# Kernel optimization log

Measured on AMD Instinct MI355X. Metric: run time of the kernel, lower is better.

Reference implementation:

```python
import jax, jax.numpy as jnp
import numpy as np

N_NODES = 100_000
N_EDGES = 1_600_000
IN_DIM = 64
OUT_DIM = 64
EPS = 1e-5


def setup_inputs() -> dict:
    key = jax.random.key(0)
    k1, k2, k3, k4, k5, k6 = jax.random.split(key, 6)
    node = jax.random.normal(k1, (N_NODES, 3), dtype=jnp.float32)
    features = jax.random.normal(k2, (N_NODES, IN_DIM), dtype=jnp.float32)
    # src column covers every node so torch.unique(edges[:,0]) == arange(N_NODES)
    src = (jnp.arange(N_EDGES, dtype=jnp.int64) % N_NODES)
    dst = jax.random.randint(k3, (N_EDGES,), 0, N_NODES, dtype=jnp.int64)
    edges = jnp.stack([src, dst], axis=1)
    # torch.nn.Linear weight: [out_dim, in_dim+3], no bias
    W = jax.random.normal(k4, (OUT_DIM, IN_DIM + 3), dtype=jnp.float32) / np.sqrt(IN_DIM + 3)
    gamma = jnp.ones((OUT_DIM,), dtype=jnp.float32)
    beta = jnp.zeros((OUT_DIM,), dtype=jnp.float32)
    return {"node": node, "features": features, "W": W, "gamma": gamma,
            "beta": beta, "edges": edges}


def reference(node, features, W, gamma, beta, edges):
    src = edges[:, 0]
    dst = edges[:, 1]
    # gather + concat: [E, in_dim + 3]
    msg = jnp.concatenate([features[dst], node[dst] - node[src]], axis=1)
    # linear (no bias): [E, out_dim]
    h = msg @ W.T
    # BatchNorm1d (training mode: biased batch statistics over E rows)
    mean = jnp.mean(h, axis=0)
    var = jnp.mean(jnp.square(h - mean), axis=0)
    h = (h - mean) * jax.lax.rsqrt(var + EPS) * gamma + beta
    h = jax.nn.relu(h)
    # scatter_reduce amax with include_self=True on a zeros tensor:
    # per-destination max, including the initial 0 (relu output >= 0 anyway)
    n = node.shape[0]
    pooled = jnp.zeros((n, h.shape[1]), dtype=features.dtype).at[src].max(h)
    return pooled
```

## Files before the change

kernel.cpp:

```cpp
#include <hip/hip_runtime.h>

#define N_NODES 100000
#define N_EDGES 1600000
#define EPS 1e-5f

typedef __bf16 bf16x8 __attribute__((ext_vector_type(8)));
typedef float  f32x4  __attribute__((ext_vector_type(4)));
typedef unsigned short u16x4 __attribute__((ext_vector_type(4)));

__device__ __forceinline__ unsigned short f2bf(float f) {
  return __builtin_bit_cast(unsigned short, static_cast<__bf16>(f));
}

__global__ __launch_bounds__(256) void prep_kernel(
    const float* __restrict__ feat, const float* __restrict__ W,
    unsigned short* __restrict__ featbf, unsigned short* __restrict__ Wbf) {
  int b = blockIdx.x, t = threadIdx.x;
  if (b < 6250) {
    int idx = (b * 256 + t) * 4;
    f32x4 v = *(const f32x4*)(feat + idx);
    u16x4 o;
    o[0] = f2bf(v[0]); o[1] = f2bf(v[1]); o[2] = f2bf(v[2]); o[3] = f2bf(v[3]);
    *(u16x4*)(featbf + idx) = o;
  } else {
    int wi = (b - 6250) * 256 + t;
    if (wi < 64 * 96) {
      int n = wi / 96, c = wi % 96;
      Wbf[wi] = (c < 67) ? f2bf(W[n * 67 + c]) : (unsigned short)0;
    }
  }
}

__global__ __launch_bounds__(256) void graph_kernel(
    const float* __restrict__ nodep, const int* __restrict__ edges,
    const unsigned short* __restrict__ featbf,
    const unsigned short* __restrict__ Wbf,
    float* __restrict__ maxv, float* __restrict__ minv,
    float* __restrict__ stats, int nwaves) {
  const int lane = threadIdx.x & 63;
  const int wave = (int)((blockIdx.x * blockDim.x + threadIdx.x) >> 6);
  const int c    = lane & 15;
  const int quad = lane >> 4;

  bf16x8 Bfrag[4][3];
#pragma unroll
  for (int t = 0; t < 4; ++t) {
    const unsigned short* wrow = Wbf + (t * 16 + c) * 96 + quad * 8;
#pragma unroll
    for (int s = 0; s < 3; ++s)
      Bfrag[t][s] = *(const bf16x8*)(wrow + s * 32);
  }

  float s1[4] = {0.f, 0.f, 0.f, 0.f};
  float s2[4] = {0.f, 0.f, 0.f, 0.f};

  for (int i = wave; i < N_NODES; i += nwaves) {
    int dst_own = 0;
    if (lane < 16) dst_own = edges[2 * (i + lane * N_NODES) + 1];
    int dst_m = __shfl(dst_own, c, 64);

    const unsigned short* frow = featbf + (size_t)dst_m * 64 + quad * 8;
    bf16x8 A0 = *(const bf16x8*)(frow);
    bf16x8 A1 = *(const bf16x8*)(frow + 32);

    bf16x8 A2;
#pragma unroll
    for (int j = 0; j < 8; ++j) A2[j] = (__bf16)0.0f;
    float nx = nodep[3 * i], ny = nodep[3 * i + 1], nz = nodep[3 * i + 2];
    if (quad == 0) {
      const float* dp = nodep + (size_t)dst_m * 3;
      A2[0] = (__bf16)(dp[0] - nx);
      A2[1] = (__bf16)(dp[1] - ny);
      A2[2] = (__bf16)(dp[2] - nz);
    }

    float mxw = 0.f, mnw = 0.f;
#pragma unroll
    for (int t = 0; t < 4; ++t) {
      f32x4 acc = {0.f, 0.f, 0.f, 0.f};
      acc = __builtin_amdgcn_mfma_f32_16x16x32_bf16(A0, Bfrag[t][0], acc, 0, 0, 0);
      acc = __builtin_amdgcn_mfma_f32_16x16x32_bf16(A1, Bfrag[t][1], acc, 0, 0, 0);
      acc = __builtin_amdgcn_mfma_f32_16x16x32_bf16(A2, Bfrag[t][2], acc, 0, 0, 0);

      float a0 = acc[0], a1 = acc[1], a2 = acc[2], a3 = acc[3];
      s1[t] += (a0 + a1) + (a2 + a3);
      s2[t] += (a0 * a0 + a1 * a1) + (a2 * a2 + a3 * a3);

      float mx = fmaxf(fmaxf(a0, a1), fmaxf(a2, a3));
      float mn = fminf(fminf(a0, a1), fminf(a2, a3));
      mx = fmaxf(mx, __shfl_xor(mx, 16, 64));
      mx = fmaxf(mx, __shfl_xor(mx, 32, 64));
      mn = fminf(mn, __shfl_xor(mn, 16, 64));
      mn = fminf(mn, __shfl_xor(mn, 32, 64));
      if (t == quad) { mxw = mx; mnw = mn; }
    }
    maxv[i * 64 + lane] = mxw;
    minv[i * 64 + lane] = mnw;
  }

#pragma unroll
  for (int t = 0; t < 4; ++t) {
    s1[t] += __shfl_xor(s1[t], 16, 64);
    s1[t] += __shfl_xor(s1[t], 32, 64);
    s2[t] += __shfl_xor(s2[t], 16, 64);
    s2[t] += __shfl_xor(s2[t], 32, 64);
  }
  float s1w = quad == 0 ? s1[0] : quad == 1 ? s1[1] : quad == 2 ? s1[2] : s1[3];
  float s2w = quad == 0 ? s2[0] : quad == 1 ? s2[1] : quad == 2 ? s2[2] : s2[3];
  stats[(size_t)lane * nwaves + wave]        = s1w;
  stats[(size_t)(64 + lane) * nwaves + wave] = s2w;
}

__global__ __launch_bounds__(256) void stats_kernel(
    const float* __restrict__ stats, const float* __restrict__ gamma,
    const float* __restrict__ beta, float* __restrict__ ss, int nwaves) {
  int d = blockIdx.x;
  int t = threadIdx.x;
  const float* r1 = stats + (size_t)d * nwaves;
  const float* r2 = stats + (size_t)(64 + d) * nwaves;
  float a = 0.f, b = 0.f;
  for (int k = t; k < nwaves; k += 256) { a += r1[k]; b += r2[k]; }
  __shared__ float l1[256], l2[256];
  l1[t] = a; l2[t] = b;
  __syncthreads();
  for (int s = 128; s > 0; s >>= 1) {
    if (t < s) { l1[t] += l1[t + s]; l2[t] += l2[t + s]; }
    __syncthreads();
  }
  if (t == 0) {
    const float inv_ne = 1.0f / (float)N_EDGES;
    float mean = l1[0] * inv_ne;
    float var  = fmaxf(l2[0] * inv_ne - mean * mean, 0.f);
    float sc   = gamma[d] * rsqrtf(var + EPS);
    ss[d]      = sc;
    ss[64 + d] = beta[d] - mean * sc;
  }
}

__global__ __launch_bounds__(256) void finalize_kernel(
    const float* __restrict__ minv, const float* __restrict__ ss,
    float* out) {
  int idx = blockIdx.x * 256 + threadIdx.x;
  int d = idx & 63;
  float sc = ss[d], sh = ss[64 + d];
  float v = (sc >= 0.f) ? out[idx] : minv[idx];
  out[idx] = fmaxf(fmaf(v, sc, sh), 0.f);
}

extern "C" void kernel_launch(void* const* d_in, const int* in_sizes, int n_in,
                              void* d_out, int out_size, void* d_ws, size_t ws_size,
                              hipStream_t stream) {
  const float* nodep = (const float*)d_in[0];
  const float* feat  = (const float*)d_in[1];
  const float* W     = (const float*)d_in[2];
  const float* gamma = (const float*)d_in[3];
  const float* beta  = (const float*)d_in[4];
  const int*   edges = (const int*)d_in[5];

  char* ws = (char*)d_ws;
  unsigned short* Wbf    = (unsigned short*)ws;
  unsigned short* featbf = (unsigned short*)(ws + 12288);
  float* minv  = (float*)(ws + 12288 + 12800000);
  float* stats = (float*)(ws + 12288 + 12800000 + 25600000);
  float* ss    = (float*)(ws + 12288 + 12800000 + 25600000 + 4194304);
  float* maxv  = (float*)d_out;

  const int nwaves = 8192;

  prep_kernel<<<6250 + 24, 256, 0, stream>>>(feat, W, featbf, Wbf);
  graph_kernel<<<nwaves / 4, 256, 0, stream>>>(nodep, edges, featbf, Wbf,
                                               maxv, minv, stats, nwaves);
  stats_kernel<<<64, 256, 0, stream>>>(stats, gamma, beta, ss, nwaves);
  finalize_kernel<<<25000, 256, 0, stream>>>(minv, ss, maxv);
}
```

Before: 178.2 us.

## Precompute per-node linear projection, then gather projected rows per edge

Uses linearity to compute W·[feat; pos] once per node (100k rows) into an fp16 table, then per edge gathers the projected row and subtracts W_pos·pos_src computed on the fly. This removes the per-edge MFMA GEMM and the separate bf16 feature conversion pass. The gather kernel also prefetches the next iteration's edge indices and reduces max/min/stats across lanes with shuffles. The risk is precision: the projection is stored in fp16 and the position difference is no longer rounded to bf16 before the multiply.

```diff
diff --git a/kernel.cpp b/kernel.cpp
--- a/kernel.cpp
+++ b/kernel.cpp
@@ -4,111 +4,152 @@
 #define N_EDGES 1600000
 #define EPS 1e-5f
 
-typedef __bf16 bf16x8 __attribute__((ext_vector_type(8)));
-typedef float  f32x4  __attribute__((ext_vector_type(4)));
-typedef unsigned short u16x4 __attribute__((ext_vector_type(4)));
-
-__device__ __forceinline__ unsigned short f2bf(float f) {
-  return __builtin_bit_cast(unsigned short, static_cast<__bf16>(f));
-}
-
-__global__ __launch_bounds__(256) void prep_kernel(
-    const float* __restrict__ feat, const float* __restrict__ W,
-    unsigned short* __restrict__ featbf, unsigned short* __restrict__ Wbf) {
-  int b = blockIdx.x, t = threadIdx.x;
-  if (b < 6250) {
-    int idx = (b * 256 + t) * 4;
-    f32x4 v = *(const f32x4*)(feat + idx);
-    u16x4 o;
-    o[0] = f2bf(v[0]); o[1] = f2bf(v[1]); o[2] = f2bf(v[2]); o[3] = f2bf(v[3]);
-    *(u16x4*)(featbf + idx) = o;
-  } else {
-    int wi = (b - 6250) * 256 + t;
-    if (wi < 64 * 96) {
-      int n = wi / 96, c = wi % 96;
-      Wbf[wi] = (c < 67) ? f2bf(W[n * 67 + c]) : (unsigned short)0;
-    }
-  }
-}
-
-__global__ __launch_bounds__(256) void graph_kernel(
+typedef __bf16    bf16x8 __attribute__((ext_vector_type(8)));
+typedef _Float16  f16x8  __attribute__((ext_vector_type(8)));
+typedef float     f32x4  __attribute__((ext_vector_type(4)));
+
+__global__ __launch_bounds__(256) void gemm_kernel(
+    const float* __restrict__ nodep, const float* __restrict__ feat,
+    const float* __restrict__ W, unsigned short* __restrict__ g) {
+  const int lane = threadIdx.x & 63;
+  const int wave = (int)((blockIdx.x * blockDim.x + threadIdx.x) >> 6);
+  const int c    = lane & 15;
+  const int quad = lane >> 4;
+  if (wave >= N_NODES / 16) return;
+
+  bf16x8 Bfrag[4][3];
+#pragma unroll
+  for (int t = 0; t < 4; ++t) {
+    const float* wrow = W + (t * 16 + c) * 67;
+#pragma unroll
+    for (int s = 0; s < 3; ++s) {
+#pragma unroll
+      for (int j = 0; j < 8; ++j) {
+        int k = s * 32 + quad * 8 + j;
+        Bfrag[t][s][j] = (k < 67) ? (__bf16)wrow[k] : (__bf16)0.0f;
+      }
+    }
+  }
+
+  const int v = wave * 16 + c;
+  const float* frow = feat + (size_t)v * 64 + quad * 8;
+  bf16x8 A0, A1;
+#pragma unroll
+  for (int j = 0; j < 8; ++j) {
+    A0[j] = (__bf16)frow[j];
+    A1[j] = (__bf16)frow[32 + j];
+  }
+  bf16x8 A2;
+#pragma unroll
+  for (int j = 0; j < 8; ++j) A2[j] = (__bf16)0.0f;
+  if (quad == 0) {
+    const float* np = nodep + (size_t)v * 3;
+    A2[0] = (__bf16)np[0];
+    A2[1] = (__bf16)np[1];
+    A2[2] = (__bf16)np[2];
+  }
+
+#pragma unroll
+  for (int t = 0; t < 4; ++t) {
+    f32x4 acc = {0.f, 0.f, 0.f, 0.f};
+    acc = __builtin_amdgcn_mfma_f32_16x16x32_bf16(A0, Bfrag[t][0], acc, 0, 0, 0);
+    acc = __builtin_amdgcn_mfma_f32_16x16x32_bf16(A1, Bfrag[t][1], acc, 0, 0, 0);
+    acc = __builtin_amdgcn_mfma_f32_16x16x32_bf16(A2, Bfrag[t][2], acc, 0, 0, 0);
+    unsigned short* gp = g + (size_t)(wave * 16 + quad * 4) * 64 + t * 16 + c;
+#pragma unroll
+    for (int r = 0; r < 4; ++r)
+      gp[r * 64] = __builtin_bit_cast(unsigned short, (_Float16)acc[r]);
+  }
+}
+
+__global__ __launch_bounds__(256) void gather_kernel(
     const float* __restrict__ nodep, const int* __restrict__ edges,
-    const unsigned short* __restrict__ featbf,
-    const unsigned short* __restrict__ Wbf,
+    const _Float16* __restrict__ g, const float* __restrict__ W,
     float* __restrict__ maxv, float* __restrict__ minv,
     float* __restrict__ stats, int nwaves) {
   const int lane = threadIdx.x & 63;
   const int wave = (int)((blockIdx.x * blockDim.x + threadIdx.x) >> 6);
-  const int c    = lane & 15;
-  const int quad = lane >> 4;
-
-  bf16x8 Bfrag[4][3];
-#pragma unroll
-  for (int t = 0; t < 4; ++t) {
-    const unsigned short* wrow = Wbf + (t * 16 + c) * 96 + quad * 8;
-#pragma unroll
-    for (int s = 0; s < 3; ++s)
-      Bfrag[t][s] = *(const bf16x8*)(wrow + s * 32);
-  }
-
-  float s1[4] = {0.f, 0.f, 0.f, 0.f};
-  float s2[4] = {0.f, 0.f, 0.f, 0.f};
-
-  for (int i = wave; i < N_NODES; i += nwaves) {
-    int dst_own = 0;
-    if (lane < 16) dst_own = edges[2 * (i + lane * N_NODES) + 1];
-    int dst_m = __shfl(dst_own, c, 64);
-
-    const unsigned short* frow = featbf + (size_t)dst_m * 64 + quad * 8;
-    bf16x8 A0 = *(const bf16x8*)(frow);
-    bf16x8 A1 = *(const bf16x8*)(frow + 32);
-
-    bf16x8 A2;
-#pragma unroll
-    for (int j = 0; j < 8; ++j) A2[j] = (__bf16)0.0f;
-    float nx = nodep[3 * i], ny = nodep[3 * i + 1], nz = nodep[3 * i + 2];
-    if (quad == 0) {
-      const float* dp = nodep + (size_t)dst_m * 3;
-      A2[0] = (__bf16)(dp[0] - nx);
-      A2[1] = (__bf16)(dp[1] - ny);
-      A2[2] = (__bf16)(dp[2] - nz);
-    }
-
-    float mxw = 0.f, mnw = 0.f;
-#pragma unroll
-    for (int t = 0; t < 4; ++t) {
-      f32x4 acc = {0.f, 0.f, 0.f, 0.f};
-      acc = __builtin_amdgcn_mfma_f32_16x16x32_bf16(A0, Bfrag[t][0], acc, 0, 0, 0);
-      acc = __builtin_amdgcn_mfma_f32_16x16x32_bf16(A1, Bfrag[t][1], acc, 0, 0, 0);
-      acc = __builtin_amdgcn_mfma_f32_16x16x32_bf16(A2, Bfrag[t][2], acc, 0, 0, 0);
-
-      float a0 = acc[0], a1 = acc[1], a2 = acc[2], a3 = acc[3];
-      s1[t] += (a0 + a1) + (a2 + a3);
-      s2[t] += (a0 * a0 + a1 * a1) + (a2 * a2 + a3 * a3);
-
-      float mx = fmaxf(fmaxf(a0, a1), fmaxf(a2, a3));
-      float mn = fminf(fminf(a0, a1), fminf(a2, a3));
-      mx = fmaxf(mx, __shfl_xor(mx, 16, 64));
-      mx = fmaxf(mx, __shfl_xor(mx, 32, 64));
-      mn = fminf(mn, __shfl_xor(mn, 16, 64));
-      mn = fminf(mn, __shfl_xor(mn, 32, 64));
-      if (t == quad) { mxw = mx; mnw = mn; }
-    }
-    maxv[i * 64 + lane] = mxw;
-    minv[i * 64 + lane] = mnw;
-  }
-
-#pragma unroll
-  for (int t = 0; t < 4; ++t) {
-    s1[t] += __shfl_xor(s1[t], 16, 64);
-    s1[t] += __shfl_xor(s1[t], 32, 64);
-    s2[t] += __shfl_xor(s2[t], 16, 64);
-    s2[t] += __shfl_xor(s2[t], 32, 64);
-  }
-  float s1w = quad == 0 ? s1[0] : quad == 1 ? s1[1] : quad == 2 ? s1[2] : s1[3];
-  float s2w = quad == 0 ? s2[0] : quad == 1 ? s2[1] : quad == 2 ? s2[2] : s2[3];
-  stats[(size_t)lane * nwaves + wave]        = s1w;
-  stats[(size_t)(64 + lane) * nwaves + wave] = s2w;
+  const int ch = lane & 7;
+  const int r0 = lane >> 3;
+
+  float wn0[8], wn1[8], wn2[8];
+#pragma unroll
+  for (int j = 0; j < 8; ++j) {
+    const float* wr = W + (ch * 8 + j) * 67 + 64;
+    wn0[j] = wr[0]; wn1[j] = wr[1]; wn2[j] = wr[2];
+  }
+
+  float sh[8], sq[8];
+#pragma unroll
+  for (int j = 0; j < 8; ++j) { sh[j] = 0.f; sq[j] = 0.f; }
+
+  int i = wave;
+  int dst_own = 0;
+  if (i < N_NODES && lane < 16) dst_own = edges[2 * (i + lane * N_NODES) + 1];
+
+  for (; i < N_NODES; i += nwaves) {
+    const int inext = i + nwaves;
+    int dst_nxt = 0;
+    if (inext < N_NODES && lane < 16)
+      dst_nxt = edges[2 * (inext + lane * N_NODES) + 1];
+
+    const int dA = __shfl(dst_own, r0, 64);
+    const int dB = __shfl(dst_own, r0 + 8, 64);
+    f16x8 va = *(const f16x8*)(g + (size_t)dA * 64 + ch * 8);
+    f16x8 vb = *(const f16x8*)(g + (size_t)dB * 64 + ch * 8);
+
+    const float nx = nodep[3 * i], ny = nodep[3 * i + 1], nz = nodep[3 * i + 2];
+
+    float mx[8], mn[8];
+#pragma unroll
+    for (int j = 0; j < 8; ++j) {
+      float cj = fmaf(wn2[j], nz, fmaf(wn1[j], ny, wn0[j] * nx));
+      float ha = (float)va[j] - cj;
+      float hb = (float)vb[j] - cj;
+      mx[j] = fmaxf(ha, hb);
+      mn[j] = fminf(ha, hb);
+      sh[j] += ha + hb;
+      sq[j] = fmaf(ha, ha, sq[j]);
+      sq[j] = fmaf(hb, hb, sq[j]);
+    }
+#pragma unroll
+    for (int j = 0; j < 8; ++j) {
+      mx[j] = fmaxf(mx[j], __shfl_xor(mx[j], 8, 64));
+      mx[j] = fmaxf(mx[j], __shfl_xor(mx[j], 16, 64));
+      mx[j] = fmaxf(mx[j], __shfl_xor(mx[j], 32, 64));
+      mn[j] = fminf(mn[j], __shfl_xor(mn[j], 8, 64));
+      mn[j] = fminf(mn[j], __shfl_xor(mn[j], 16, 64));
+      mn[j] = fminf(mn[j], __shfl_xor(mn[j], 32, 64));
+    }
+    if (lane < 8) {
+      f32x4 a = {mx[0], mx[1], mx[2], mx[3]};
+      f32x4 b = {mx[4], mx[5], mx[6], mx[7]};
+      *(f32x4*)(maxv + (size_t)i * 64 + ch * 8)     = a;
+      *(f32x4*)(maxv + (size_t)i * 64 + ch * 8 + 4) = b;
+      f32x4 p = {mn[0], mn[1], mn[2], mn[3]};
+      f32x4 q = {mn[4], mn[5], mn[6], mn[7]};
+      *(f32x4*)(minv + (size_t)i * 64 + ch * 8)     = p;
+      *(f32x4*)(minv + (size_t)i * 64 + ch * 8 + 4) = q;
+    }
+    dst_own = dst_nxt;
+  }
+
+#pragma unroll
+  for (int j = 0; j < 8; ++j) {
+    sh[j] += __shfl_xor(sh[j], 8, 64);
+    sh[j] += __shfl_xor(sh[j], 16, 64);
+    sh[j] += __shfl_xor(sh[j], 32, 64);
+    sq[j] += __shfl_xor(sq[j], 8, 64);
+    sq[j] += __shfl_xor(sq[j], 16, 64);
+    sq[j] += __shfl_xor(sq[j], 32, 64);
+  }
+  if (lane < 8) {
+#pragma unroll
+    for (int j = 0; j < 8; ++j) {
+      stats[(size_t)(ch * 8 + j) * nwaves + wave]      = sh[j];
+      stats[(size_t)(64 + ch * 8 + j) * nwaves + wave] = sq[j];
+    }
+  }
 }
 
 __global__ __launch_bounds__(256) void stats_kernel(
@@ -158,18 +199,17 @@
   const int*   edges = (const int*)d_in[5];
 
   char* ws = (char*)d_ws;
-  unsigned short* Wbf    = (unsigned short*)ws;
-  unsigned short* featbf = (unsigned short*)(ws + 12288);
-  float* minv  = (float*)(ws + 12288 + 12800000);
-  float* stats = (float*)(ws + 12288 + 12800000 + 25600000);
-  float* ss    = (float*)(ws + 12288 + 12800000 + 25600000 + 4194304);
+  unsigned short* g = (unsigned short*)ws;
+  float* minv  = (float*)(ws + 12800000);
+  float* stats = (float*)(ws + 12800000 + 25600000);
+  float* ss    = (float*)(ws + 12800000 + 25600000 + 4194304);
   float* maxv  = (float*)d_out;
 
   const int nwaves = 8192;
 
-  prep_kernel<<<6250 + 24, 256, 0, stream>>>(feat, W, featbf, Wbf);
-  graph_kernel<<<nwaves / 4, 256, 0, stream>>>(nodep, edges, featbf, Wbf,
-                                               maxv, minv, stats, nwaves);
+  gemm_kernel<<<1563, 256, 0, stream>>>(nodep, feat, W, g);
+  gather_kernel<<<2048, 256, 0, stream>>>(nodep, edges, (const _Float16*)g, W,
+                                          maxv, minv, stats, nwaves);
   stats_kernel<<<64, 256, 0, stream>>>(stats, gamma, beta, ss, nwaves);
   finalize_kernel<<<25000, 256, 0, stream>>>(minv, ss, maxv);
 }
```

Result: slower. 198.3 us (+11.3%).
